# Kernel optimization log

Hardware: AMD Instinct MI355X
Metric: run time of the kernel (lower is better)

Reference implementation:

```python
import jax, jax.numpy as jnp
import numpy as np

N, E, IN, OUT = 50000, 1600000, 128, 64
BN_EPS = 1e-5


def setup_inputs() -> dict:
    key = jax.random.key(0)
    ks = jax.random.split(key, 12)
    x = jax.random.normal(ks[0], (N, IN), jnp.float32)
    edge_index = jax.random.randint(ks[1], (2, E), 0, N)
    node_embeddings = jax.random.normal(ks[2], (N, OUT), jnp.float32)
    W = jax.random.normal(ks[3], (OUT, IN), jnp.float32) / np.sqrt(IN).astype(np.float32)
    att_i = jax.random.normal(ks[4], (OUT,), jnp.float32) * 0.1
    att_j = jax.random.normal(ks[5], (OUT,), jnp.float32) * 0.1
    att_em_i = jax.random.normal(ks[6], (OUT,), jnp.float32) * 0.1
    att_em_j = jax.random.normal(ks[7], (OUT,), jnp.float32) * 0.1
    bias = jax.random.normal(ks[8], (OUT,), jnp.float32) * 0.01
    gamma = jnp.ones((OUT,), jnp.float32)
    beta = jnp.zeros((OUT,), jnp.float32)
    return dict(x=x, edge_index=edge_index, node_embeddings=node_embeddings, W=W,
                att_i=att_i, att_j=att_j, att_em_i=att_em_i, att_em_j=att_em_j,
                bias=bias, gamma=gamma, beta=beta)


def _segment_softmax(logits, seg, num_segments):
    # numerically stable softmax over edges grouped by destination node
    m = jax.ops.segment_max(logits, seg, num_segments=num_segments)
    e = jnp.exp(logits - m[seg])
    s = jax.ops.segment_sum(e, seg, num_segments=num_segments)
    return e / (s[seg] + 1e-16)


def reference(x, edge_index, node_embeddings, W, att_i, att_j, att_em_i, att_em_j,
              bias, gamma, beta):
    n = x.shape[0]
    h = x @ W.T                                  # [N, OUT] linear projection
    src, dst = edge_index[0], edge_index[1]      # j -> i (source_to_target)
    # per-node attention scalars first (N*OUT work), then gather scalars per edge
    # (same math as gathering [E,OUT] keys, far less memory traffic)
    a_i = h @ att_i + node_embeddings @ att_em_i  # [N]
    a_j = h @ att_j + node_embeddings @ att_em_j  # [N]
    logits = jax.nn.leaky_relu(a_i[dst] + a_j[src], 0.2)   # [E]
    alpha = _segment_softmax(logits, dst, n)                # [E]
    agg = jax.ops.segment_sum(h[src] * alpha[:, None], dst, num_segments=n)  # [N, OUT]
    out = agg + bias
    # BatchNorm1d (training mode: batch stats, biased variance) + ReLU
    mean = out.mean(0)
    var = out.var(0)
    y = gamma * (out - mean) * jax.lax.rsqrt(var + BN_EPS) + beta
    return jax.nn.relu(y)
```

## Files before the change

### kernel.cpp

```cpp
#include <hip/hip_runtime.h>
#include <climits>

#define NN 50000
#define EE 1600000
#define DIN 128
#define DOUT 64
#define BN_EPS 1e-5f

#define NPB 32
#define NB  1563
#define CAPB 1536
#define NCB 49
#define CAPC 35200
#define KA1_WGS 512
#define KA1_CHUNK (EE / KA1_WGS)
#define KA2_SPLIT 16

__global__ void k0_init(int* gcur, int* gcurC, float* colsum, float* colsq) {
    int i = blockIdx.x * blockDim.x + threadIdx.x;
    if (i < NB + 8) gcur[i] = 0;
    if (i < NCB) gcurC[i] = 0;
    if (i < DOUT) { colsum[i] = 0.f; colsq[i] = 0.f; }
}

__global__ void k1_gemm(const float* __restrict__ x, const float* __restrict__ W,
                        const float* __restrict__ ne,
                        const float* __restrict__ atti, const float* __restrict__ attj,
                        const float* __restrict__ atemi, const float* __restrict__ atemj,
                        float* __restrict__ h, float* __restrict__ a_i, float* __restrict__ a_j) {
    const int l = threadIdx.x & 63;
    const int wv = threadIdx.x >> 6;
    const int gw = blockIdx.x * (blockDim.x >> 6) + wv;
    const int nw = gridDim.x * (blockDim.x >> 6);

    float4 w4[32];
    const float4* Wv = (const float4*)(W + l * DIN);
#pragma unroll
    for (int j = 0; j < 32; ++j) w4[j] = Wv[j];

    const float ai_l = atti[l], aj_l = attj[l], emi_l = atemi[l], emj_l = atemj[l];

    for (int n = gw; n < NN; n += nw) {
        const float4* xv = (const float4*)(x + n * DIN);
        float acc = 0.f;
#pragma unroll
        for (int j = 0; j < 32; ++j) {
            float4 xx = xv[j];
            acc += w4[j].x * xx.x + w4[j].y * xx.y + w4[j].z * xx.z + w4[j].w * xx.w;
        }
        float nev = ne[n * DOUT + l];
        float v1 = acc * ai_l + nev * emi_l;
        float v2 = acc * aj_l + nev * emj_l;
#pragma unroll
        for (int d = 32; d >= 1; d >>= 1) {
            v1 += __shfl_xor(v1, d);
            v2 += __shfl_xor(v2, d);
        }
        h[n * DOUT + l] = acc;
        if (l == 0) { a_i[n] = v1; a_j[n] = v2; }
    }
}

__global__ void __launch_bounds__(256) kA1_coarse(const int* __restrict__ ei,
                                                  int* __restrict__ gcurC,
                                                  unsigned int* __restrict__ coarse) {
    __shared__ int hist[NCB];
    __shared__ int base_l[NCB];
    __shared__ unsigned int recs[KA1_CHUNK];
    const int t = threadIdx.x;
    if (t < NCB) hist[t] = 0;
    __syncthreads();
    const int e0 = blockIdx.x * KA1_CHUNK;
    for (int e = e0 + t; e < e0 + KA1_CHUNK; e += 256) {
        int src = ei[e];
        int dst = ei[EE + e];
        atomicAdd(&hist[dst >> 10], 1);
        recs[e - e0] = (unsigned)src | ((unsigned)dst << 16);
    }
    __syncthreads();
    if (t < NCB) {
        int c = hist[t];
        base_l[t] = c > 0 ? atomicAdd(&gcurC[t], c) : 0;
        hist[t] = 0;
    }
    __syncthreads();
    for (int e = e0 + t; e < e0 + KA1_CHUNK; e += 256) {
        unsigned r = recs[e - e0];
        int cb = (r >> 16) >> 10;
        int pos = base_l[cb] + atomicAdd(&hist[cb], 1);
        coarse[cb * CAPC + pos] = r;
    }
}

__global__ void __launch_bounds__(256) kA2_fine(const unsigned int* __restrict__ coarse,
                                                const int* __restrict__ gcurC,
                                                int* __restrict__ gcur,
                                                unsigned int* __restrict__ binned) {
    __shared__ int hist[32];
    __shared__ int base_l[32];
    __shared__ unsigned int recs[CAPC / KA2_SPLIT + 64];
    const int c = blockIdx.x >> 4;
    const int q = blockIdx.x & 15;
    const int len = gcurC[c];
    const int start = (len * q) / KA2_SPLIT;
    const int end = (len * (q + 1)) / KA2_SPLIT;
    const int t = threadIdx.x;
    if (t < 32) hist[t] = 0;
    __syncthreads();
    const unsigned int* cb = coarse + c * CAPC;
    for (int i = start + t; i < end; i += 256) {
        unsigned r = cb[i];
        recs[i - start] = r;
        atomicAdd(&hist[(r >> 21) & 31], 1);
    }
    __syncthreads();
    if (t < 32) {
        int n = hist[t];
        base_l[t] = n > 0 ? atomicAdd(&gcur[c * 32 + t], n) : 0;
        hist[t] = 0;
    }
    __syncthreads();
    for (int i = start + t; i < end; i += 256) {
        unsigned r = recs[i - start];
        int fb = (r >> 21) & 31;
        int pos = base_l[fb] + atomicAdd(&hist[fb], 1);
        binned[(c * 32 + fb) * CAPB + pos] = (r & 0xffffu) | (((r >> 16) & 31u) << 16);
    }
}

__global__ void __launch_bounds__(256) kB_agg(const unsigned int* __restrict__ binned,
                                              const int* __restrict__ gcur,
                                              const float* __restrict__ h,
                                              const float* __restrict__ a_i,
                                              const float* __restrict__ a_j,
                                              const float* __restrict__ bias,
                                              float* __restrict__ out_pre,
                                              float* __restrict__ colsum,
                                              float* __restrict__ colsq) {
    __shared__ float agg[NPB * DOUT];
    __shared__ float s_l[NPB];
    __shared__ float ai_l[NPB];
    const int b = blockIdx.x;
    const int node0 = b * NPB;
    const int nlocal = min(NPB, NN - node0);
    const int t = threadIdx.x;
    const int l = t & 63, wv = t >> 6;
    const float bias_l = bias[l];

    for (int i = t; i < NPB * DOUT; i += 256) agg[i] = 0.f;
    if (t < NPB) {
        s_l[t] = 0.f;
        ai_l[t] = (t < nlocal) ? a_i[node0 + t] : 0.f;
    }
    __syncthreads();

    const int cnt = gcur[b];
    const unsigned int* bin = binned + b * CAPB;

    for (int base = wv * 64; base < cnt; base += 256) {
        const int kk = min(64, cnt - base);
        unsigned r = (l < kk) ? bin[base + l] : 0u;
        int src = r & 0xffffu;
        int dl = (r >> 16) & 31;
        float ev = 0.f;
        if (l < kk) {
            float lg = ai_l[dl] + a_j[src];
            lg = lg > 0.f ? lg : 0.2f * lg;
            ev = __expf(lg);
            atomicAdd(&s_l[dl], ev);
        }
        int evi = __float_as_int(ev);
        if (kk == 64) {
            float hv[64];
#pragma unroll
            for (int u = 0; u < 64; ++u) {
                int sK = __builtin_amdgcn_readlane(src, u);
                hv[u] = h[(sK << 6) + l];
            }
            __builtin_amdgcn_sched_barrier(0);
#pragma unroll
            for (int u = 0; u < 64; ++u) {
                int dK = __builtin_amdgcn_readlane(dl, u);
                float eK = __int_as_float(__builtin_amdgcn_readlane(evi, u));
                atomicAdd(&agg[(dK << 6) + l], eK * hv[u]);
            }
        } else {
            for (int k = 0; k < kk; ++k) {
                int sK = __builtin_amdgcn_readlane(src, k);
                int dK = __builtin_amdgcn_readlane(dl, k);
                float eK = __int_as_float(__builtin_amdgcn_readlane(evi, k));
                float hvv = h[(sK << 6) + l];
                atomicAdd(&agg[(dK << 6) + l], eK * hvv);
            }
        }
    }
    __syncthreads();

    float bsum = 0.f, bsq = 0.f;
    for (int j = wv; j < nlocal; j += 4) {
        float v = agg[j * 64 + l] / (s_l[j] + 1e-16f) + bias_l;
        out_pre[(node0 + j) * 64 + l] = v;
        bsum += v;
        bsq += v * v;
    }
    __syncthreads();
    agg[wv * 64 + l] = bsum;
    agg[256 + wv * 64 + l] = bsq;
    __syncthreads();
    if (wv == 0) {
        float ts = agg[l] + agg[64 + l] + agg[128 + l] + agg[192 + l];
        float tq = agg[256 + l] + agg[320 + l] + agg[384 + l] + agg[448 + l];
        atomicAdd(&colsum[l], ts);
        atomicAdd(&colsq[l], tq);
    }
}

__global__ void k6_coef(const float* __restrict__ colsum, const float* __restrict__ colsq,
                        const float* __restrict__ gamma, const float* __restrict__ beta,
                        float* __restrict__ scale, float* __restrict__ shift) {
    int c = threadIdx.x;
    if (c < DOUT) {
        float mean = colsum[c] * (1.f / NN);
        float var = colsq[c] * (1.f / NN) - mean * mean;
        float inv = rsqrtf(var + BN_EPS);
        float sc = gamma[c] * inv;
        scale[c] = sc;
        shift[c] = beta[c] - mean * sc;
    }
}

__global__ void k7_apply(const float4* __restrict__ out_pre,
                         const float4* __restrict__ scale, const float4* __restrict__ shift,
                         float4* __restrict__ y) {
    const int n4 = NN * DOUT / 4;
    int tid = blockIdx.x * blockDim.x + threadIdx.x;
    int stride = gridDim.x * blockDim.x;
    for (int i = tid; i < n4; i += stride) {
        float4 o = out_pre[i];
        int c = i & 15;
        float4 sc = scale[c], sh = shift[c];
        float4 r;
        r.x = fmaxf(o.x * sc.x + sh.x, 0.f);
        r.y = fmaxf(o.y * sc.y + sh.y, 0.f);
        r.z = fmaxf(o.z * sc.z + sh.z, 0.f);
        r.w = fmaxf(o.w * sc.w + sh.w, 0.f);
        y[i] = r;
    }
}

extern "C" void kernel_launch(void* const* d_in, const int* in_sizes, int n_in,
                              void* d_out, int out_size, void* d_ws, size_t ws_size,
                              hipStream_t stream) {
    const float* x      = (const float*)d_in[0];
    const int*   ei     = (const int*)d_in[1];
    const float* ne     = (const float*)d_in[2];
    const float* W      = (const float*)d_in[3];
    const float* att_i  = (const float*)d_in[4];
    const float* att_j  = (const float*)d_in[5];
    const float* atemi  = (const float*)d_in[6];
    const float* atemj  = (const float*)d_in[7];
    const float* bias   = (const float*)d_in[8];
    const float* gamma  = (const float*)d_in[9];
    const float* beta   = (const float*)d_in[10];
    float* out = (float*)d_out;

    char* w = (char*)d_ws;
    size_t off = 0;
    auto alloc = [&](size_t bytes) -> void* {
        void* p = w + off;
        off = (off + bytes + 255) & ~(size_t)255;
        return p;
    };
    float*        h       = (float*)alloc((size_t)NN * DOUT * 4);
    float*        out_pre = (float*)alloc((size_t)NN * DOUT * 4);
    unsigned int* binned  = (unsigned int*)alloc((size_t)NB * CAPB * 4);
    float*        a_i     = (float*)alloc((size_t)NN * 4);
    float*        a_j     = (float*)alloc((size_t)NN * 4);
    int*          gcur    = (int*)alloc((size_t)(NB + 8) * 4);
    int*          gcurC   = (int*)alloc((size_t)NCB * 4);
    float*        colsum  = (float*)alloc(DOUT * 4);
    float*        colsq   = (float*)alloc(DOUT * 4);
    float*        scale   = (float*)alloc(DOUT * 4);
    float*        shift   = (float*)alloc(DOUT * 4);
    unsigned int* coarse  = (unsigned int*)out_pre;

    k0_init<<<(NB + 255 + 8) / 256, 256, 0, stream>>>(gcur, gcurC, colsum, colsq);
    k1_gemm<<<1024, 256, 0, stream>>>(x, W, ne, att_i, att_j, atemi, atemj, h, a_i, a_j);
    kA1_coarse<<<KA1_WGS, 256, 0, stream>>>(ei, gcurC, coarse);
    kA2_fine<<<NCB * KA2_SPLIT, 256, 0, stream>>>(coarse, gcurC, gcur, binned);
    kB_agg<<<NB, 256, 0, stream>>>(binned, gcur, h, a_i, a_j, bias, out_pre, colsum, colsq);
    k6_coef<<<1, 64, 0, stream>>>(colsum, colsq, gamma, beta, scale, shift);
    k7_apply<<<1024, 256, 0, stream>>>((const float4*)out_pre, (const float4*)scale,
                                       (const float4*)shift, (float4*)out);
}
```

Measured before the change: 878.3 us.

## Switch kB_agg to edge-per-lane aggregation with padded shared rows

The aggregation loop changes from feature-per-lane (a wave broadcasts each edge via readlane and lanes gather one column of h) to edge-per-lane. Each lane now loads its source row of h as 16 float4 vectors and atomically adds all 64 weighted features into its destination's shared-memory row. Shared rows are padded to a stride of 68 floats to spread bank conflicts when lanes hit different destinations. This gives wide per-lane loads in place of 64 scattered scalar loads. The cost is heavier register use, uncoalesced row loads across lanes, and more contention on shared atomics when lanes share a destination.

```diff
diff --git a/kernel.cpp b/kernel.cpp
--- a/kernel.cpp
+++ b/kernel.cpp
@@ -10,6 +10,7 @@
 #define NPB 32
 #define NB  1563
 #define CAPB 1536
+#define ASTR 68
 #define NCB 49
 #define CAPC 35200
 #define KA1_WGS 512
@@ -137,7 +138,7 @@
                                               float* __restrict__ out_pre,
                                               float* __restrict__ colsum,
                                               float* __restrict__ colsq) {
-    __shared__ float agg[NPB * DOUT];
+    __shared__ float agg[NPB * ASTR];
     __shared__ float s_l[NPB];
     __shared__ float ai_l[NPB];
     const int b = blockIdx.x;
@@ -147,7 +148,7 @@
     const int l = t & 63, wv = t >> 6;
     const float bias_l = bias[l];
 
-    for (int i = t; i < NPB * DOUT; i += 256) agg[i] = 0.f;
+    for (int i = t; i < NPB * ASTR; i += 256) agg[i] = 0.f;
     if (t < NPB) {
         s_l[t] = 0.f;
         ai_l[t] = (t < nlocal) ? a_i[node0 + t] : 0.f;
@@ -159,38 +160,26 @@
 
     for (int base = wv * 64; base < cnt; base += 256) {
         const int kk = min(64, cnt - base);
-        unsigned r = (l < kk) ? bin[base + l] : 0u;
-        int src = r & 0xffffu;
-        int dl = (r >> 16) & 31;
-        float ev = 0.f;
         if (l < kk) {
+            unsigned r = bin[base + l];
+            int src = r & 0xffffu;
+            int dl = (r >> 16) & 31;
             float lg = ai_l[dl] + a_j[src];
             lg = lg > 0.f ? lg : 0.2f * lg;
-            ev = __expf(lg);
+            float ev = __expf(lg);
             atomicAdd(&s_l[dl], ev);
-        }
-        int evi = __float_as_int(ev);
-        if (kk == 64) {
-            float hv[64];
-#pragma unroll
-            for (int u = 0; u < 64; ++u) {
-                int sK = __builtin_amdgcn_readlane(src, u);
-                hv[u] = h[(sK << 6) + l];
-            }
-            __builtin_amdgcn_sched_barrier(0);
-#pragma unroll
-            for (int u = 0; u < 64; ++u) {
-                int dK = __builtin_amdgcn_readlane(dl, u);
-                float eK = __int_as_float(__builtin_amdgcn_readlane(evi, u));
-                atomicAdd(&agg[(dK << 6) + l], eK * hv[u]);
-            }
-        } else {
-            for (int k = 0; k < kk; ++k) {
-                int sK = __builtin_amdgcn_readlane(src, k);
-                int dK = __builtin_amdgcn_readlane(dl, k);
-                float eK = __int_as_float(__builtin_amdgcn_readlane(evi, k));
-                float hvv = h[(sK << 6) + l];
-                atomicAdd(&agg[(dK << 6) + l], eK * hvv);
+
+            const float4* hrow = (const float4*)(h + (src << 6));
+            float* arow = agg + dl * ASTR;
+            float4 v[16];
+#pragma unroll
+            for (int c = 0; c < 16; ++c) v[c] = hrow[c];
+#pragma unroll
+            for (int c = 0; c < 16; ++c) {
+                atomicAdd(&arow[c * 4 + 0], ev * v[c].x);
+                atomicAdd(&arow[c * 4 + 1], ev * v[c].y);
+                atomicAdd(&arow[c * 4 + 2], ev * v[c].z);
+                atomicAdd(&arow[c * 4 + 3], ev * v[c].w);
             }
         }
     }
@@ -198,7 +187,7 @@
 
     float bsum = 0.f, bsq = 0.f;
     for (int j = wv; j < nlocal; j += 4) {
-        float v = agg[j * 64 + l] / (s_l[j] + 1e-16f) + bias_l;
+        float v = agg[j * ASTR + l] / (s_l[j] + 1e-16f) + bias_l;
         out_pre[(node0 + j) * 64 + l] = v;
         bsum += v;
         bsq += v * v;
```

New measurement: 881.6 us. No clear change (+0.4%).
